# Optimization experiments

Measured on AMD Instinct MI355X. Metric: run time of the kernel, lower is better.

The kernel has to match this reference:

```python
import jax, jax.numpy as jnp
import numpy as np


def setup_inputs() -> dict:
    key = jax.random.key(0)
    k1, k2, k3 = jax.random.split(key, 3)
    B, S, K, N = 4, 2048, 4096, 4096
    x = jax.random.normal(k1, (B, S, K), dtype=jnp.float16)
    # int8 weight codes in [-128, 127]
    w_int8 = jax.random.randint(k2, (N, K), -128, 128, dtype=jnp.int32).astype(jnp.int8)
    # per-output-row weight scale (positive, smallish like abs-max/127 of fp weights)
    weight_scale = (jax.random.uniform(k3, (N,), dtype=jnp.float32) + 0.5) * 0.01
    matmul_out_scale = jnp.full((1,), 1.0 / 1024.0, dtype=jnp.float32)
    return {"x": x, "w_int8": w_int8, "weight_scale": weight_scale,
            "matmul_out_scale": matmul_out_scale}


def reference(x, w_int8, weight_scale, matmul_out_scale):
    B, S, K = x.shape
    xf = x.astype(jnp.float32)
    # dynamic per-token symmetric int8 quantization (TOKEN_INT8_127)
    x_scales = jnp.max(jnp.abs(xf), axis=-1, keepdims=True) / 127.0  # [B,S,1] float32
    x_int8 = jnp.clip(jnp.round(xf / x_scales), -128, 127).astype(jnp.int8)
    x_scales_h = x_scales[..., 0].astype(jnp.float16)  # [B,S]
    y = jnp.einsum('mk,nk->mn', x_int8.reshape(-1, K), w_int8,
                   preferred_element_type=jnp.int32).astype(jnp.float32)
    y = y.reshape(B, S, -1)
    y = (y * matmul_out_scale[0]).astype(jnp.float16)
    # fp16 * fp32 -> fp32 (matches torch type promotion); per-row and per-token dequant
    out = y * weight_scale * x_scales_h[:, :, None]
    return out
```

## Files before the change

### kernel.cpp

```cpp
#include <hip/hip_runtime.h>
#include <hip/hip_fp16.h>
#include <stdint.h>

typedef int v4i __attribute__((ext_vector_type(4)));

#define GLOAD_LDS16(g, l) __builtin_amdgcn_global_load_lds(                  \
    (const __attribute__((address_space(1))) void*)(g),                      \
    (__attribute__((address_space(3))) void*)(l), 16, 0, 0)

#define XQ_OFF 0u
#define XS_OFF 33554432u
#define W8_OFF 33570816u

__device__ inline bool x_is_f32(const void* xin) {
  const uint32_t* xw = (const uint32_t*)xin;
  bool ok = true;
  #pragma unroll
  for (int i = 0; i < 16; ++i) ok &= ((xw[i] & 0x1FFFu) == 0u);
  return ok;
}
__device__ inline bool w_is_i32(const void* win) {
  const int* wi = (const int*)win;
  bool ok = true;
  #pragma unroll
  for (int i = 0; i < 16; ++i) ok &= (wi[i] >= -128 && wi[i] <= 127);
  return ok;
}

#define RW_BLOCKS 1024

__global__ __launch_bounds__(256) void prologue(
    const void* __restrict__ xin, const void* __restrict__ win,
    int8_t* __restrict__ xq, __half* __restrict__ xs,
    int8_t* __restrict__ w8, int K, int M, int wtotal)
{
  const int tid = threadIdx.x;

  if (blockIdx.x >= (unsigned)M) {
    const bool as32 = w_is_i32(win);
    const int bid  = blockIdx.x - M;
    const int gtid = bid * 256 + tid;
    const int nthr = RW_BLOCKS * 256;
    if (as32) {
      const int4* w4 = (const int4*)win;
      uint32_t* dst = (uint32_t*)w8;
      const int n4 = wtotal >> 2;
      for (int i = gtid; i < n4; i += nthr) {
        int4 v = w4[i];
        dst[i] = (uint32_t)(v.x & 255) | ((uint32_t)(v.y & 255) << 8) |
                 ((uint32_t)(v.z & 255) << 16) | ((uint32_t)(v.w & 255) << 24);
      }
    } else {
      const uint4* src = (const uint4*)win;
      uint4* dst = (uint4*)w8;
      const int n16 = wtotal >> 4;
      for (int i = gtid; i < n16; i += nthr) dst[i] = src[i];
    }
    return;
  }

  const bool xf32 = x_is_f32(xin);
  const int row  = blockIdx.x;
  const int lane = tid & 63;
  const int wv   = tid >> 6;
  const size_t base = (size_t)row * (size_t)K;
  __shared__ float wmax[4];

  if (xf32 && K == 4096) {
    const float4* x4 = (const float4*)((const float*)xin + base);
    float4 v[4];
    #pragma unroll
    for (int i = 0; i < 4; ++i) v[i] = x4[i * 256 + tid];
    float mx = 0.0f;
    #pragma unroll
    for (int i = 0; i < 4; ++i)
      mx = fmaxf(mx, fmaxf(fmaxf(fabsf(v[i].x), fabsf(v[i].y)),
                           fmaxf(fabsf(v[i].z), fabsf(v[i].w))));
    #pragma unroll
    for (int off = 32; off; off >>= 1) mx = fmaxf(mx, __shfl_xor(mx, off, 64));
    if (lane == 0) wmax[wv] = mx;
    __syncthreads();
    const float scale =
        fmaxf(fmaxf(wmax[0], wmax[1]), fmaxf(wmax[2], wmax[3])) / 127.0f;
    if (tid == 0) xs[row] = __float2half(scale);
    uint32_t* q = (uint32_t*)(xq + base);
    #pragma unroll
    for (int i = 0; i < 4; ++i) {
      float f[4] = {v[i].x, v[i].y, v[i].z, v[i].w};
      uint32_t p = 0;
      #pragma unroll
      for (int j = 0; j < 4; ++j) {
        float r = fminf(127.0f, fmaxf(-128.0f, rintf(f[j] / scale)));
        p |= ((uint32_t)((int)r & 255)) << (8 * j);
      }
      q[i * 256 + tid] = p;
    }
    return;
  }

  float mx = 0.0f;
  if (xf32) {
    const float* x = (const float*)xin + base;
    for (int k = tid * 4; k < K; k += 256 * 4) {
      float4 v = *(const float4*)(x + k);
      mx = fmaxf(mx, fmaxf(fmaxf(fabsf(v.x), fabsf(v.y)),
                           fmaxf(fabsf(v.z), fabsf(v.w))));
    }
  } else {
    const __half* x = (const __half*)xin + base;
    for (int k = tid * 8; k < K; k += 256 * 8) {
      uint4 u = *(const uint4*)(x + k);
      const __half* hp = (const __half*)&u;
      #pragma unroll
      for (int j = 0; j < 8; ++j) mx = fmaxf(mx, fabsf(__half2float(hp[j])));
    }
  }
  #pragma unroll
  for (int off = 32; off; off >>= 1) mx = fmaxf(mx, __shfl_xor(mx, off, 64));
  if (lane == 0) wmax[wv] = mx;
  __syncthreads();
  const float scale =
      fmaxf(fmaxf(wmax[0], wmax[1]), fmaxf(wmax[2], wmax[3])) / 127.0f;
  if (tid == 0) xs[row] = __float2half(scale);

  for (int k = tid * 8; k < K; k += 256 * 8) {
    float f[8];
    if (xf32) {
      const float* x = (const float*)xin + base;
      float4 a = *(const float4*)(x + k);
      float4 b = *(const float4*)(x + k + 4);
      f[0]=a.x; f[1]=a.y; f[2]=a.z; f[3]=a.w; f[4]=b.x; f[5]=b.y; f[6]=b.z; f[7]=b.w;
    } else {
      const __half* x = (const __half*)xin + base;
      uint4 u = *(const uint4*)(x + k);
      const __half* hp = (const __half*)&u;
      #pragma unroll
      for (int j = 0; j < 8; ++j) f[j] = __half2float(hp[j]);
    }
    uint32_t p0 = 0, p1 = 0;
    #pragma unroll
    for (int j = 0; j < 4; ++j) {
      float r = fminf(127.0f, fmaxf(-128.0f, rintf(f[j] / scale)));
      p0 |= ((uint32_t)((int)r & 255)) << (8 * j);
    }
    #pragma unroll
    for (int j = 0; j < 4; ++j) {
      float r = fminf(127.0f, fmaxf(-128.0f, rintf(f[4 + j] / scale)));
      p1 |= ((uint32_t)((int)r & 255)) << (8 * j);
    }
    uint2 st; st.x = p0; st.y = p1;
    *(uint2*)(xq + base + k) = st;
  }
}

__global__ __launch_bounds__(512, 2) void gemm_w8a8(
    const int8_t* __restrict__ xq, const int8_t* __restrict__ wq,
    const __half* __restrict__ xs, const float* __restrict__ wscale,
    const float* __restrict__ mos, float* __restrict__ out,
    int M, int N, int K)
{
  __shared__ int8_t sA[4][256 * 64];
  __shared__ int8_t sB[4][256 * 64];

  const int tid  = threadIdx.x;
  const int lane = tid & 63;
  const int w    = tid >> 6;
  const int wr   = w >> 2;
  const int wc   = w & 3;
  const int lr   = lane & 15;
  const int lk   = lane >> 4;

  int L = blockIdx.x;
  const int nwg = gridDim.x;
  if ((nwg & 7) == 0) L = (L & 7) * (nwg >> 3) + (L >> 3);
  const int ntn = N >> 8;
  const int bn = (L % ntn) << 8;
  const int bm = (L / ntn) << 8;

  v4i acc[8][4];
  #pragma unroll
  for (int i = 0; i < 8; ++i)
    #pragma unroll
    for (int j = 0; j < 4; ++j) {
      v4i z = {0, 0, 0, 0};
      acc[i][j] = z;
    }

  auto stageA = [&](int kt, int buf) {
    const int k0 = kt << 6;
    #pragma unroll
    for (int i = 0; i < 2; ++i) {
      const int li = i * 512 + tid;
      const int r  = li >> 2;
      const int p  = li & 3;
      const int sc = p ^ ((r >> 1) & 3);
      GLOAD_LDS16(xq + (size_t)(bm + r) * K + k0 + (sc << 4),
                  &sA[buf][(i * 512 + (w << 6)) << 4]);
    }
  };
  auto stageB = [&](int kt, int buf) {
    const int k0 = kt << 6;
    #pragma unroll
    for (int i = 0; i < 2; ++i) {
      const int li = i * 512 + tid;
      const int r  = li >> 2;
      const int p  = li & 3;
      const int sc = p ^ ((r >> 1) & 3);
      GLOAD_LDS16(wq + (size_t)(bn + r) * K + k0 + (sc << 4),
                  &sB[buf][(i * 512 + (w << 6)) << 4]);
    }
  };

  const int rowA0 = (wr << 7) + lr;
  const int aoff  = rowA0 * 64 + ((lk ^ ((rowA0 >> 1) & 3)) << 4);
  const int rowB0 = (wc << 6) + lr;
  const int boff  = rowB0 * 64 + ((lk ^ ((rowB0 >> 1) & 3)) << 4);

  const int nt = K >> 6;

  stageA(0, 0); stageB(0, 0);
  stageA(1, 1); stageB(1, 1);
  asm volatile("s_waitcnt vmcnt(4)" ::: "memory");
  __builtin_amdgcn_s_barrier();

  v4i a0[8], b0[4], a1[8], b1[4];
  #pragma unroll
  for (int j = 0; j < 8; ++j) a0[j] = *(const v4i*)(&sA[0][aoff + j * 1024]);
  #pragma unroll
  for (int j = 0; j < 4; ++j) b0[j] = *(const v4i*)(&sB[0][boff + j * 1024]);

#define ITER(T, CA, CB, NA, NB)                                              \
  {                                                                          \
    const bool ds = (T) + 2 < nt;                                            \
    if (ds) { stageA((T) + 2, ((T) + 2) & 3);                                \
              stageB((T) + 2, ((T) + 2) & 3); }                              \
    asm volatile("s_waitcnt lgkmcnt(0)" ::: "memory");                       \
    __builtin_amdgcn_s_setprio(1);                                           \
    _Pragma("unroll")                                                        \
    for (int mi = 0; mi < 4; ++mi)                                           \
      _Pragma("unroll")                                                      \
      for (int ni = 0; ni < 4; ++ni)                                         \
        acc[mi][ni] = __builtin_amdgcn_mfma_i32_16x16x64_i8(                 \
            CA[mi], CB[ni], acc[mi][ni], 0, 0, 0);                           \
    __builtin_amdgcn_s_setprio(0);                                           \
    if ((T) + 1 < nt) {                                                      \
      if (ds) { asm volatile("s_waitcnt vmcnt(8)" ::: "memory"); }           \
      else    { asm volatile("s_waitcnt vmcnt(0)" ::: "memory"); }           \
      __builtin_amdgcn_s_barrier();                                          \
      const int8_t* An = sA[((T) + 1) & 3];                                  \
      const int8_t* Bn = sB[((T) + 1) & 3];                                  \
      _Pragma("unroll")                                                      \
      for (int j = 0; j < 8; ++j)                                            \
        NA[j] = *(const v4i*)(An + aoff + j * 1024);                         \
      _Pragma("unroll")                                                      \
      for (int j = 0; j < 4; ++j)                                            \
        NB[j] = *(const v4i*)(Bn + boff + j * 1024);                         \
    }                                                                        \
    __builtin_amdgcn_s_setprio(1);                                           \
    _Pragma("unroll")                                                        \
    for (int mi = 0; mi < 4; ++mi)                                           \
      _Pragma("unroll")                                                      \
      for (int ni = 0; ni < 4; ++ni)                                         \
        acc[4 + mi][ni] = __builtin_amdgcn_mfma_i32_16x16x64_i8(             \
            CA[4 + mi], CB[ni], acc[4 + mi][ni], 0, 0, 0);                   \
    __builtin_amdgcn_s_setprio(0);                                           \
  }

  #pragma unroll 1
  for (int t = 0; t < nt; t += 2) {
    ITER(t,     a0, b0, a1, b1)
    ITER(t + 1, a1, b1, a0, b0)
  }
#undef ITER

  const float s_out = mos[0];
  #pragma unroll
  for (int ni = 0; ni < 4; ++ni) {
    const int n_g = bn + (wc << 6) + ni * 16 + lr;
    const float wsc = wscale[n_g];
    #pragma unroll
    for (int mi = 0; mi < 8; ++mi) {
      #pragma unroll
      for (int j = 0; j < 4; ++j) {
        const int m_g = bm + (wr << 7) + mi * 16 + lk * 4 + j;
        const float y = __half2float(__float2half((float)acc[mi][ni][j] * s_out));
        out[(size_t)m_g * N + n_g] = (y * wsc) * __half2float(xs[m_g]);
      }
    }
  }
}

extern "C" void kernel_launch(void* const* d_in, const int* in_sizes, int n_in,
                              void* d_out, int out_size, void* d_ws, size_t ws_size,
                              hipStream_t stream) {
  const void*  x      = d_in[0];
  const void*  win    = d_in[1];
  const float* wscale = (const float*)d_in[2];
  const float* mos    = (const float*)d_in[3];
  float*       out    = (float*)d_out;

  const int N = in_sizes[2];
  const int K = in_sizes[1] / N;
  const int M = in_sizes[0] / K;

  int8_t* xq = (int8_t*)d_ws + XQ_OFF;
  __half* xs = (__half*)((char*)d_ws + XS_OFF);
  int8_t* w8 = (int8_t*)d_ws + W8_OFF;

  prologue<<<M + RW_BLOCKS, 256, 0, stream>>>(x, win, xq, xs, w8, K, M, N * K);

  gemm_w8a8<<<dim3((M >> 8) * (N >> 8)), 512, 0, stream>>>(
      xq, w8, xs, wscale, mos, out, M, N, K);
}
```

Baseline: 194.0 us.

## Load weight operand directly into registers and double-buffer only activations in LDS

The B (weight) tile is no longer staged through LDS. Each lane loads its weight fragments straight from global memory into registers, double-buffered across k-tiles. The A tile now uses a 128-wide K step with a two-buffer LDS ring and an 8-way XOR swizzle. The aim is to cut LDS traffic and shared-memory footprint, at the cost of uncoalesced 16-byte global loads for B, more register pressure, and a full vmcnt(0) wait at the start of each tile, which reduces overlap.

New measurement: 398.5 us. 2.05x slower.

```diff
diff --git a/kernel.cpp b/kernel.cpp
--- a/kernel.cpp
+++ b/kernel.cpp
@@ -159,8 +159,7 @@
     const float* __restrict__ mos, float* __restrict__ out,
     int M, int N, int K)
 {
-  __shared__ int8_t sA[4][256 * 64];
-  __shared__ int8_t sB[4][256 * 64];
+  __shared__ int8_t sA[2][256 * 128];
 
   const int tid  = threadIdx.x;
   const int lane = tid & 63;
@@ -187,91 +186,95 @@
     }
 
   auto stageA = [&](int kt, int buf) {
-    const int k0 = kt << 6;
-    #pragma unroll
-    for (int i = 0; i < 2; ++i) {
+    const int k0 = kt << 7;
+    #pragma unroll
+    for (int i = 0; i < 4; ++i) {
       const int li = i * 512 + tid;
-      const int r  = li >> 2;
-      const int p  = li & 3;
-      const int sc = p ^ ((r >> 1) & 3);
+      const int r  = li >> 3;
+      const int p  = li & 7;
+      const int sc = p ^ (r & 7);
       GLOAD_LDS16(xq + (size_t)(bm + r) * K + k0 + (sc << 4),
                   &sA[buf][(i * 512 + (w << 6)) << 4]);
     }
   };
-  auto stageB = [&](int kt, int buf) {
-    const int k0 = kt << 6;
-    #pragma unroll
-    for (int i = 0; i < 2; ++i) {
-      const int li = i * 512 + tid;
-      const int r  = li >> 2;
-      const int p  = li & 3;
-      const int sc = p ^ ((r >> 1) & 3);
-      GLOAD_LDS16(wq + (size_t)(bn + r) * K + k0 + (sc << 4),
-                  &sB[buf][(i * 512 + (w << 6)) << 4]);
-    }
-  };
 
   const int rowA0 = (wr << 7) + lr;
-  const int aoff  = rowA0 * 64 + ((lk ^ ((rowA0 >> 1) & 3)) << 4);
-  const int rowB0 = (wc << 6) + lr;
-  const int boff  = rowB0 * 64 + ((lk ^ ((rowB0 >> 1) & 3)) << 4);
-
-  const int nt = K >> 6;
-
-  stageA(0, 0); stageB(0, 0);
-  stageA(1, 1); stageB(1, 1);
-  asm volatile("s_waitcnt vmcnt(4)" ::: "memory");
+  const int aoff0 = rowA0 * 128 + ((lk ^ (lr & 7)) << 4);
+  const int aoff1 = aoff0 ^ 64;
+
+  const int8_t* wrow = wq + (size_t)(bn + (wc << 6) + lr) * K + (lk << 4);
+  const size_t nstep = (size_t)16 * (size_t)K;
+
+  const int nt = K >> 7;
+
+  v4i b0A[4], b1A[4], b0B[4], b1B[4];
+  stageA(0, 0);
+  #pragma unroll
+  for (int ni = 0; ni < 4; ++ni) b0A[ni] = *(const v4i*)(wrow + ni * nstep);
+  #pragma unroll
+  for (int ni = 0; ni < 4; ++ni) b1A[ni] = *(const v4i*)(wrow + ni * nstep + 64);
+  asm volatile("s_waitcnt vmcnt(0)" ::: "memory");
   __builtin_amdgcn_s_barrier();
 
-  v4i a0[8], b0[4], a1[8], b1[4];
-  #pragma unroll
-  for (int j = 0; j < 8; ++j) a0[j] = *(const v4i*)(&sA[0][aoff + j * 1024]);
-  #pragma unroll
-  for (int j = 0; j < 4; ++j) b0[j] = *(const v4i*)(&sB[0][boff + j * 1024]);
-
-#define ITER(T, CA, CB, NA, NB)                                              \
-  {                                                                          \
-    const bool ds = (T) + 2 < nt;                                            \
-    if (ds) { stageA((T) + 2, ((T) + 2) & 3);                                \
-              stageB((T) + 2, ((T) + 2) & 3); }                              \
-    asm volatile("s_waitcnt lgkmcnt(0)" ::: "memory");                       \
+#define MFMA16(BASE, AV, BV)                                                 \
     __builtin_amdgcn_s_setprio(1);                                           \
     _Pragma("unroll")                                                        \
-    for (int mi = 0; mi < 4; ++mi)                                           \
+    for (int j = 0; j < 4; ++j)                                              \
       _Pragma("unroll")                                                      \
       for (int ni = 0; ni < 4; ++ni)                                         \
-        acc[mi][ni] = __builtin_amdgcn_mfma_i32_16x16x64_i8(                 \
-            CA[mi], CB[ni], acc[mi][ni], 0, 0, 0);                           \
-    __builtin_amdgcn_s_setprio(0);                                           \
-    if ((T) + 1 < nt) {                                                      \
-      if (ds) { asm volatile("s_waitcnt vmcnt(8)" ::: "memory"); }           \
-      else    { asm volatile("s_waitcnt vmcnt(0)" ::: "memory"); }           \
-      __builtin_amdgcn_s_barrier();                                          \
-      const int8_t* An = sA[((T) + 1) & 3];                                  \
-      const int8_t* Bn = sB[((T) + 1) & 3];                                  \
-      _Pragma("unroll")                                                      \
-      for (int j = 0; j < 8; ++j)                                            \
-        NA[j] = *(const v4i*)(An + aoff + j * 1024);                         \
-      _Pragma("unroll")                                                      \
-      for (int j = 0; j < 4; ++j)                                            \
-        NB[j] = *(const v4i*)(Bn + boff + j * 1024);                         \
-    }                                                                        \
-    __builtin_amdgcn_s_setprio(1);                                           \
-    _Pragma("unroll")                                                        \
-    for (int mi = 0; mi < 4; ++mi)                                           \
+        acc[(BASE) + j][ni] = __builtin_amdgcn_mfma_i32_16x16x64_i8(         \
+            AV[j], BV[ni], acc[(BASE) + j][ni], 0, 0, 0);                    \
+    __builtin_amdgcn_s_setprio(0);
+
+#define TILE(T, BC0, BC1, BN0, BN1)                                          \
+  {                                                                          \
+    const int buf = (T) & 1;                                                 \
+    const int8_t* Ab = sA[buf];                                              \
+    const bool ds = (T) + 1 < nt;                                            \
+    const int k0n = ((T) + 1) << 7;                                          \
+    v4i a0[4], a1[4];                                                        \
+    asm volatile("s_waitcnt vmcnt(0)" ::: "memory");   \
+    _Pragma("unroll")                                                        \
+    for (int j = 0; j < 4; ++j) a0[j] = *(const v4i*)(Ab + aoff0 + j * 2048);\
+    if (ds) stageA((T) + 1, buf ^ 1);                                        \
+    asm volatile("s_waitcnt lgkmcnt(0)" ::: "memory");                       \
+    MFMA16(0, a0, BC0)                                                       \
+    _Pragma("unroll")                                                        \
+    for (int j = 0; j < 4; ++j)                                              \
+      a1[j] = *(const v4i*)(Ab + aoff0 + 8192 + j * 2048);                   \
+    if (ds) {                                                                \
       _Pragma("unroll")                                                      \
       for (int ni = 0; ni < 4; ++ni)                                         \
-        acc[4 + mi][ni] = __builtin_amdgcn_mfma_i32_16x16x64_i8(             \
-            CA[4 + mi], CB[ni], acc[4 + mi][ni], 0, 0, 0);                   \
-    __builtin_amdgcn_s_setprio(0);                                           \
+        BN0[ni] = *(const v4i*)(wrow + ni * nstep + k0n);                    \
+    }                                                                        \
+    asm volatile("s_waitcnt lgkmcnt(0)" ::: "memory");                       \
+    MFMA16(4, a1, BC0)                                                       \
+    _Pragma("unroll")                                                        \
+    for (int j = 0; j < 4; ++j) a0[j] = *(const v4i*)(Ab + aoff1 + j * 2048);\
+    if (ds) {                                                                \
+      _Pragma("unroll")                                                      \
+      for (int ni = 0; ni < 4; ++ni)                                         \
+        BN1[ni] = *(const v4i*)(wrow + ni * nstep + k0n + 64);               \
+    }                                                                        \
+    asm volatile("s_waitcnt lgkmcnt(0)" ::: "memory");                       \
+    MFMA16(0, a0, BC1)                                                       \
+    _Pragma("unroll")                                                        \
+    for (int j = 0; j < 4; ++j)                                              \
+      a1[j] = *(const v4i*)(Ab + aoff1 + 8192 + j * 2048);                   \
+    asm volatile("s_waitcnt lgkmcnt(0)" ::: "memory");                       \
+    MFMA16(4, a1, BC1)                                                       \
+            \
+    asm volatile("s_waitcnt vmcnt(8)" ::: "memory");                         \
+    __builtin_amdgcn_s_barrier();                                            \
   }
 
   #pragma unroll 1
   for (int t = 0; t < nt; t += 2) {
-    ITER(t,     a0, b0, a1, b1)
-    ITER(t + 1, a1, b1, a0, b0)
-  }
-#undef ITER
+    TILE(t,     b0A, b1A, b0B, b1B)
+    TILE(t + 1, b0B, b1B, b0A, b1A)
+  }
+#undef TILE
+#undef MFMA16
 
   const float s_out = mos[0];
   #pragma unroll
```

## Restructure int8 GEMM main loop into barrier-phased half-tile load/MFMA schedule

Applied to the files above, without the earlier changes.

Replaces the register double-buffered main loop, which preloaded full A and B fragments for the next tile, with a four-phase schedule per pair of k-tiles. Each phase loads half of the A fragments from LDS, issues part of the next tile's global-to-LDS staging, and then runs 16 MFMAs, with barriers between phases. The aim is to cut register pressure, since the next tile's fragments are no longer held while computing, possibly allowing better occupancy and interleaving of loads with MFMAs. The cost is many more workgroup barriers per iteration, and LDS read latency is exposed before each MFMA group instead of being hidden behind the previous compute.

After: 203.5 us. +4.9%, slower.

```diff
diff --git a/kernel.cpp b/kernel.cpp
--- a/kernel.cpp
+++ b/kernel.cpp
@@ -218,60 +218,72 @@
 
   const int nt = K >> 6;
 
-  stageA(0, 0); stageB(0, 0);
-  stageA(1, 1); stageB(1, 1);
-  asm volatile("s_waitcnt vmcnt(4)" ::: "memory");
-  __builtin_amdgcn_s_barrier();
-
-  v4i a0[8], b0[4], a1[8], b1[4];
-  #pragma unroll
-  for (int j = 0; j < 8; ++j) a0[j] = *(const v4i*)(&sA[0][aoff + j * 1024]);
-  #pragma unroll
-  for (int j = 0; j < 4; ++j) b0[j] = *(const v4i*)(&sB[0][boff + j * 1024]);
-
-#define ITER(T, CA, CB, NA, NB)                                              \
-  {                                                                          \
-    const bool ds = (T) + 2 < nt;                                            \
-    if (ds) { stageA((T) + 2, ((T) + 2) & 3);                                \
-              stageB((T) + 2, ((T) + 2) & 3); }                              \
-    asm volatile("s_waitcnt lgkmcnt(0)" ::: "memory");                       \
+#define MFMA16(BASE, AV, BV)                                                 \
     __builtin_amdgcn_s_setprio(1);                                           \
     _Pragma("unroll")                                                        \
     for (int mi = 0; mi < 4; ++mi)                                           \
       _Pragma("unroll")                                                      \
       for (int ni = 0; ni < 4; ++ni)                                         \
-        acc[mi][ni] = __builtin_amdgcn_mfma_i32_16x16x64_i8(                 \
-            CA[mi], CB[ni], acc[mi][ni], 0, 0, 0);                           \
-    __builtin_amdgcn_s_setprio(0);                                           \
-    if ((T) + 1 < nt) {                                                      \
-      if (ds) { asm volatile("s_waitcnt vmcnt(8)" ::: "memory"); }           \
-      else    { asm volatile("s_waitcnt vmcnt(0)" ::: "memory"); }           \
-      __builtin_amdgcn_s_barrier();                                          \
-      const int8_t* An = sA[((T) + 1) & 3];                                  \
-      const int8_t* Bn = sB[((T) + 1) & 3];                                  \
-      _Pragma("unroll")                                                      \
-      for (int j = 0; j < 8; ++j)                                            \
-        NA[j] = *(const v4i*)(An + aoff + j * 1024);                         \
-      _Pragma("unroll")                                                      \
-      for (int j = 0; j < 4; ++j)                                            \
-        NB[j] = *(const v4i*)(Bn + boff + j * 1024);                         \
-    }                                                                        \
-    __builtin_amdgcn_s_setprio(1);                                           \
-    _Pragma("unroll")                                                        \
-    for (int mi = 0; mi < 4; ++mi)                                           \
-      _Pragma("unroll")                                                      \
-      for (int ni = 0; ni < 4; ++ni)                                         \
-        acc[4 + mi][ni] = __builtin_amdgcn_mfma_i32_16x16x64_i8(             \
-            CA[4 + mi], CB[ni], acc[4 + mi][ni], 0, 0, 0);                   \
-    __builtin_amdgcn_s_setprio(0);                                           \
-  }
+        acc[(BASE) + mi][ni] = __builtin_amdgcn_mfma_i32_16x16x64_i8(        \
+            AV[mi], BV[ni], acc[(BASE) + mi][ni], 0, 0, 0);                  \
+    __builtin_amdgcn_s_setprio(0);
+
+  stageA(0, 0); stageB(0, 0);
+  stageA(1, 1); stageB(1, 1);
+  asm volatile("s_waitcnt vmcnt(4)" ::: "memory");
+  __builtin_amdgcn_s_barrier();
 
   #pragma unroll 1
   for (int t = 0; t < nt; t += 2) {
-    ITER(t,     a0, b0, a1, b1)
-    ITER(t + 1, a1, b1, a0, b0)
-  }
-#undef ITER
+    const bool ds2 = (t + 2 < nt);
+    const bool ds3 = (t + 3 < nt);
+    const int8_t* A0 = sA[t & 3];
+    const int8_t* B0 = sB[t & 3];
+    const int8_t* A1 = sA[(t + 1) & 3];
+    const int8_t* B1 = sB[(t + 1) & 3];
+    v4i a[4], bf0[4], bf1[4];
+
+    #pragma unroll
+    for (int j = 0; j < 4; ++j) bf0[j] = *(const v4i*)(B0 + boff + j * 1024);
+    #pragma unroll
+    for (int j = 0; j < 4; ++j) a[j]   = *(const v4i*)(A0 + aoff + j * 1024);
+    if (ds2) stageA(t + 2, (t + 2) & 3);
+    __builtin_amdgcn_s_barrier();
+    asm volatile("s_waitcnt lgkmcnt(0)" ::: "memory");
+    MFMA16(0, a, bf0)
+    __builtin_amdgcn_s_barrier();
+
+    #pragma unroll
+    for (int j = 0; j < 4; ++j) a[j] = *(const v4i*)(A0 + aoff + 4096 + j * 1024);
+    if (ds2) stageB(t + 2, (t + 2) & 3);
+    __builtin_amdgcn_s_barrier();
+    asm volatile("s_waitcnt lgkmcnt(0)" ::: "memory");
+    MFMA16(4, a, bf0)
+    if (ds2) { asm volatile("s_waitcnt vmcnt(4)" ::: "memory"); }
+    else     { asm volatile("s_waitcnt vmcnt(0)" ::: "memory"); }
+    __builtin_amdgcn_s_barrier();
+
+    #pragma unroll
+    for (int j = 0; j < 4; ++j) bf1[j] = *(const v4i*)(B1 + boff + j * 1024);
+    #pragma unroll
+    for (int j = 0; j < 4; ++j) a[j]   = *(const v4i*)(A1 + aoff + j * 1024);
+    if (ds3) stageA(t + 3, (t + 3) & 3);
+    __builtin_amdgcn_s_barrier();
+    asm volatile("s_waitcnt lgkmcnt(0)" ::: "memory");
+    MFMA16(0, a, bf1)
+    __builtin_amdgcn_s_barrier();
+
+    #pragma unroll
+    for (int j = 0; j < 4; ++j) a[j] = *(const v4i*)(A1 + aoff + 4096 + j * 1024);
+    if (ds3) stageB(t + 3, (t + 3) & 3);
+    __builtin_amdgcn_s_barrier();
+    asm volatile("s_waitcnt lgkmcnt(0)" ::: "memory");
+    MFMA16(4, a, bf1)
+    if (ds3) { asm volatile("s_waitcnt vmcnt(4)" ::: "memory"); }
+    else     { asm volatile("s_waitcnt vmcnt(0)" ::: "memory"); }
+    __builtin_amdgcn_s_barrier();
+  }
+#undef MFMA16
 
   const float s_out = mos[0];
   #pragma unroll
```
